# Kernel optimization log

Measured on AMD Instinct MI355X. Metric: run time of the kernel, lower is better.

The kernel has to match this reference:

```python
import jax, jax.numpy as jnp
import numpy as np

N_HEADS = 8
BUCKET = 64
EPS = 1e-4


def setup_inputs() -> dict:
    key = jax.random.key(0)
    ks = jax.random.split(key, 8)
    B, S, D = 4, 8192, 1024
    s = 1.0 / np.sqrt(D).astype(np.float32)
    x = jax.random.normal(ks[0], (B, S, D), dtype=jnp.float32)
    W_hash = jax.random.normal(ks[1], (D, 2 * N_HEADS), dtype=jnp.float32) * s
    W_q = jax.random.normal(ks[2], (D, D), dtype=jnp.float32) * s
    b_q = jax.random.normal(ks[3], (D,), dtype=jnp.float32) * 0.01
    W_v = jax.random.normal(ks[4], (D, D), dtype=jnp.float32) * s
    b_v = jax.random.normal(ks[5], (D,), dtype=jnp.float32) * 0.01
    W_o = jax.random.normal(ks[6], (D, D), dtype=jnp.float32) * s
    b_o = jax.random.normal(ks[7], (D,), dtype=jnp.float32) * 0.01
    return {"x": x, "W_hash": W_hash, "W_q": W_q, "b_q": b_q,
            "W_v": W_v, "b_v": b_v, "W_o": W_o, "b_o": b_o}


def reference(x, W_hash, W_q, b_q, W_v, b_v, W_o, b_o):
    B, S, D = x.shape
    H, dh = N_HEADS, D // N_HEADS
    nb = S // BUCKET  # number of LSH buckets per head

    # --- LSH hash: one angle per head, sort tokens by angle (per head) ---
    h = (x @ W_hash).reshape(B, S, H, 2)
    angles = h[..., 0] / (h[..., 1] + EPS)          # [B, S, H]
    idx = jnp.argsort(angles.transpose(0, 2, 1), axis=2)  # [B, H, S]

    # --- projections (shared_qk: k uses the same projection as q) ---
    q = x @ W_q + b_q
    k = q
    v = x @ W_v + b_v

    def to_heads(t):
        return t.reshape(B, S, H, dh).transpose(0, 2, 1, 3)  # [B, H, S, dh]

    qh, kh, vh = to_heads(q), to_heads(k), to_heads(v)

    gather = lambda t: jnp.take_along_axis(t, idx[..., None], axis=2)
    qs = gather(qh).reshape(B, H, nb, BUCKET, dh)
    ks = gather(kh).reshape(B, H, nb, BUCKET, dh)
    vs = gather(vh).reshape(B, H, nb, BUCKET, dh)

    # --- bucketed local attention ---
    scale = 1.0 / np.sqrt(dh).astype(np.float32)
    scores = jnp.einsum('bhnid,bhnjd->bhnij', qs, ks) * scale
    attn = jax.nn.softmax(scores, axis=-1)
    o = jnp.einsum('bhnij,bhnjd->bhnid', attn, vs).reshape(B, H, S, dh)

    # --- unsort back to original token order ---
    inv = jnp.argsort(idx, axis=2)                  # inverse permutation [B, H, S]
    o = jnp.take_along_axis(o, inv[..., None], axis=2)
    o = o.transpose(0, 2, 1, 3).reshape(B, S, D)
    return o @ W_o + b_o
```

## Files before the change

kernel.cpp:

```cpp
#include <hip/hip_runtime.h>

typedef unsigned short u16;
using short8 = __attribute__((ext_vector_type(8))) short;
using u16x8  = __attribute__((ext_vector_type(8))) unsigned short;
using f32x4  = __attribute__((ext_vector_type(4))) float;

#define B_   4
#define S_   8192
#define D_   1024
#define H_   8
#define DH_  128
#define NB_  128
#define M_   (B_ * S_)

static __device__ __forceinline__ float bf2f(u16 u) {
  union { unsigned int i; float f; } v; v.i = ((unsigned int)u) << 16; return v.f;
}
static __device__ __forceinline__ u16 f2bf(float f) {
  unsigned int x = __float_as_uint(f);
  unsigned int r = (x + 0x7fffu + ((x >> 16) & 1u)) >> 16;
  return (u16)r;
}
static __device__ __forceinline__ f32x4 mfma16(short8 a, short8 b, f32x4 c) {
  return __builtin_amdgcn_mfma_f32_16x16x32_bf16(a, b, c, 0, 0, 0);
}
static __device__ __forceinline__ void gload16(const u16* g, u16* l) {
  __builtin_amdgcn_global_load_lds(
      (const __attribute__((address_space(1))) void*)g,
      (__attribute__((address_space(3))) void*)l, 16, 0, 0);
}

__global__ __launch_bounds__(256) void cvt_k(const float* __restrict__ src,
                                             u16* __restrict__ dst) {
  const size_t i = ((size_t)blockIdx.x * 256 + threadIdx.x) * 8;
  const f32x4 a = *(const f32x4*)(src + i);
  const f32x4 b = *(const f32x4*)(src + i + 4);
  u16x8 r;
  r[0] = f2bf(a[0]); r[1] = f2bf(a[1]); r[2] = f2bf(a[2]); r[3] = f2bf(a[3]);
  r[4] = f2bf(b[0]); r[5] = f2bf(b[1]); r[6] = f2bf(b[2]); r[7] = f2bf(b[3]);
  *(u16x8*)(dst + i) = r;
}

__global__ __launch_bounds__(256) void transpose_k(const float* __restrict__ src,
                                                   u16* __restrict__ dst) {
  __shared__ float tile[32][33];
  const int bx = blockIdx.x * 32, by = blockIdx.y * 32;
  const int tx = threadIdx.x, ty = threadIdx.y;
#pragma unroll
  for (int i = ty; i < 32; i += 8) tile[i][tx] = src[(size_t)(by + i) * D_ + bx + tx];
  __syncthreads();
#pragma unroll
  for (int i = ty; i < 32; i += 8) dst[(size_t)(bx + i) * D_ + by + tx] = f2bf(tile[tx][i]);
}

__global__ __launch_bounds__(128) void angles_k(const float* __restrict__ x,
                                                const float* __restrict__ Wh,
                                                float* __restrict__ angles) {
  __shared__ float wsh[D_ * 16];
  const int tid = threadIdx.x;
  for (int i = tid; i < D_ * 16; i += 128) wsh[i] = Wh[i];
  __syncthreads();
  const int token = blockIdx.x * 128 + tid;
  const float* xr = x + (size_t)token * D_;
  f32x4 acc4[4];
#pragma unroll
  for (int i = 0; i < 4; i++) acc4[i] = 0.0f;
  for (int d0 = 0; d0 < D_; d0 += 4) {
    const f32x4 pk = *(const f32x4*)(xr + d0);
#pragma unroll
    for (int j = 0; j < 4; j++) {
      const float xv = pk[j];
      const f32x4* wr = (const f32x4*)&wsh[(d0 + j) * 16];
#pragma unroll
      for (int c4 = 0; c4 < 4; c4++) acc4[c4] += wr[c4] * xv;
    }
  }
  const int b = token >> 13, s = token & (S_ - 1);
#pragma unroll
  for (int h = 0; h < H_; h++) {
    const float num = acc4[h >> 1][(h & 1) * 2 + 0];
    const float den = acc4[h >> 1][(h & 1) * 2 + 1];
    angles[(size_t)(b * H_ + h) * S_ + s] = num / (den + 1e-4f);
  }
}

__global__ __launch_bounds__(1024) void sort_k(const float* __restrict__ angles,
                                               int* __restrict__ idx) {
  __shared__ float key[S_];
  __shared__ int   val[S_];
  const float* a = angles + (size_t)blockIdx.x * S_;
  const int tid = threadIdx.x;
  for (int i = tid; i < S_; i += 1024) { key[i] = a[i]; val[i] = i; }
  __syncthreads();
  for (int k = 2; k <= S_; k <<= 1) {
    for (int j = k >> 1; j > 0; j >>= 1) {
      for (int i = tid; i < S_; i += 1024) {
        const int ixj = i ^ j;
        if (ixj > i) {
          const float ki = key[i], kj = key[ixj];
          const bool up = (i & k) == 0;
          if (up ? (ki > kj) : (ki < kj)) {
            key[i] = kj; key[ixj] = ki;
            const int t = val[i]; val[i] = val[ixj]; val[ixj] = t;
          }
        }
      }
      __syncthreads();
    }
  }
  int* out = idx + (size_t)blockIdx.x * S_;
  for (int i = tid; i < S_; i += 1024) out[i] = val[i];
}

template <bool CF32>
__global__ __launch_bounds__(256) void gemm_bt(const u16* __restrict__ A,
                                               const u16* __restrict__ Bt,
                                               const float* __restrict__ bias,
                                               void* __restrict__ Cv,
                                               int M, int N, int K) {
  __shared__ __attribute__((aligned(16))) u16 As[128][32];
  __shared__ __attribute__((aligned(16))) u16 Bs[128][32];
  const int tid = threadIdx.x;
  const int wave = tid >> 6, lane = tid & 63;
  const int l16 = lane & 15, quad = lane >> 4;
  const int m0 = blockIdx.x * 128, n0 = blockIdx.y * 128;
  const int wm = wave >> 1, wn = wave & 1;
  const int srow = lane >> 2;
  const int scol = (lane & 3) * 8;

  const u16* Ag0 = A  + (size_t)(m0 + wave * 16 + srow) * K + scol;
  const u16* Ag1 = A  + (size_t)(m0 + 64 + wave * 16 + srow) * K + scol;
  const u16* Bg0 = Bt + (size_t)(n0 + wave * 16 + srow) * K + scol;
  const u16* Bg1 = Bt + (size_t)(n0 + 64 + wave * 16 + srow) * K + scol;
  u16* AsD0 = &As[wave * 16 + srow][scol];
  u16* AsD1 = &As[64 + wave * 16 + srow][scol];
  u16* BsD0 = &Bs[wave * 16 + srow][scol];
  u16* BsD1 = &Bs[64 + wave * 16 + srow][scol];

  f32x4 acc[4][4];
#pragma unroll
  for (int i = 0; i < 4; i++)
#pragma unroll
    for (int j = 0; j < 4; j++) acc[i][j] = 0.0f;

  for (int k0 = 0; k0 < K; k0 += 32) {
    __syncthreads();
    gload16(Ag0 + k0, AsD0);
    gload16(Ag1 + k0, AsD1);
    gload16(Bg0 + k0, BsD0);
    gload16(Bg1 + k0, BsD1);
    __syncthreads();
    short8 af[4], bfr[4];
#pragma unroll
    for (int i = 0; i < 4; i++)
      af[i] = *(const short8*)&As[wm * 64 + i * 16 + l16][quad * 8];
#pragma unroll
    for (int i = 0; i < 4; i++)
      bfr[i] = *(const short8*)&Bs[wn * 64 + i * 16 + l16][quad * 8];
#pragma unroll
    for (int mi = 0; mi < 4; mi++)
#pragma unroll
      for (int ni = 0; ni < 4; ni++)
        acc[mi][ni] = mfma16(af[mi], bfr[ni], acc[mi][ni]);
  }

#pragma unroll
  for (int ni = 0; ni < 4; ni++) {
    const int col = n0 + wn * 64 + ni * 16 + l16;
    const float bv = bias[col];
#pragma unroll
    for (int mi = 0; mi < 4; mi++) {
      const int rowb = m0 + wm * 64 + mi * 16 + quad * 4;
#pragma unroll
      for (int r = 0; r < 4; r++) {
        const float cv = acc[mi][ni][r] + bv;
        if (CF32) ((float*)Cv)[(size_t)(rowb + r) * N + col] = cv;
        else      ((u16*)Cv)[(size_t)(rowb + r) * N + col] = f2bf(cv);
      }
    }
  }
}

__global__ __launch_bounds__(256) void attn_k(const u16* __restrict__ qbuf,
                                              const u16* __restrict__ vbuf,
                                              const int* __restrict__ idx,
                                              u16* __restrict__ obuf) {
  __shared__ u16  Qs[64][136];
  __shared__ u16  Vt[128][72];
  __shared__ float Ss[64][65];
  __shared__ u16  Ps[64][72];
  __shared__ int  tids[64];
  const int b = blockIdx.z, h = blockIdx.y, n = blockIdx.x;
  const int tid = threadIdx.x;
  const int lane = tid & 63, wave = tid >> 6;
  const int l16 = lane & 15, quad = lane >> 4;

  if (tid < 64) tids[tid] = idx[(size_t)(b * H_ + h) * S_ + n * 64 + tid];
  __syncthreads();

  {
    const int i = tid & 63, seg = tid >> 6;
    const size_t rowoff = (size_t)(b * S_ + tids[i]) * D_ + h * DH_ + seg * 32;
    const u16* qr = qbuf + rowoff;
    const u16* vr = vbuf + rowoff;
#pragma unroll
    for (int c = 0; c < 32; c += 8)
      *(u16x8*)&Qs[i][seg * 32 + c] = *(const u16x8*)(qr + c);
#pragma unroll
    for (int c = 0; c < 32; c += 8) {
      u16x8 pv = *(const u16x8*)(vr + c);
#pragma unroll
      for (int j = 0; j < 8; j++) Vt[seg * 32 + c + j][i] = pv[j];
    }
  }
  __syncthreads();

  f32x4 sacc[4];
#pragma unroll
  for (int i = 0; i < 4; i++) sacc[i] = 0.0f;
#pragma unroll
  for (int k0 = 0; k0 < DH_; k0 += 32) {
    const short8 af = *(const short8*)&Qs[wave * 16 + l16][k0 + quad * 8];
#pragma unroll
    for (int ni = 0; ni < 4; ni++) {
      const short8 bfr = *(const short8*)&Qs[ni * 16 + l16][k0 + quad * 8];
      sacc[ni] = mfma16(af, bfr, sacc[ni]);
    }
  }
  const float scale = 0.08838834764831845f;
#pragma unroll
  for (int ni = 0; ni < 4; ni++)
#pragma unroll
    for (int r = 0; r < 4; r++)
      Ss[wave * 16 + quad * 4 + r][ni * 16 + l16] = sacc[ni][r] * scale;
  __syncthreads();

  {
    const int row = tid >> 2, part = tid & 3;
    float e[16]; float mx = -3.0e38f;
#pragma unroll
    for (int c = 0; c < 16; c++) { e[c] = Ss[row][part * 16 + c]; mx = fmaxf(mx, e[c]); }
    mx = fmaxf(mx, __shfl_xor(mx, 1));
    mx = fmaxf(mx, __shfl_xor(mx, 2));
    float sum = 0.f;
#pragma unroll
    for (int c = 0; c < 16; c++) { e[c] = __expf(e[c] - mx); sum += e[c]; }
    sum += __shfl_xor(sum, 1);
    sum += __shfl_xor(sum, 2);
    const float inv = 1.0f / sum;
#pragma unroll
    for (int c = 0; c < 16; c++) Ps[row][part * 16 + c] = f2bf(e[c] * inv);
  }
  __syncthreads();

  f32x4 oacc[8];
#pragma unroll
  for (int i = 0; i < 8; i++) oacc[i] = 0.0f;
#pragma unroll
  for (int k0 = 0; k0 < 64; k0 += 32) {
    const short8 pf = *(const short8*)&Ps[wave * 16 + l16][k0 + quad * 8];
#pragma unroll
    for (int nt = 0; nt < 8; nt++) {
      const short8 vf = *(const short8*)&Vt[nt * 16 + l16][k0 + quad * 8];
      oacc[nt] = mfma16(pf, vf, oacc[nt]);
    }
  }

  u16 (*Os)[128] = (u16(*)[128])&Ss[0][0];
#pragma unroll
  for (int r = 0; r < 4; r++) {
    const int m = wave * 16 + quad * 4 + r;
    const int swz = ((m >> 2) & 3) * 32;
#pragma unroll
    for (int nt = 0; nt < 8; nt++) Os[m][(nt * 16 + l16) ^ swz] = f2bf(oacc[nt][r]);
  }
  __syncthreads();

  {
    const int row = tid >> 2, c0 = (tid & 3) * 32;
    const int swz = ((row >> 2) & 3) * 32;
    u16* orow = obuf + (size_t)(b * S_ + tids[row]) * D_ + h * DH_ + c0;
#pragma unroll
    for (int c = 0; c < 32; c += 8)
      *(u16x8*)(orow + c) = *(const u16x8*)&Os[row][(c0 + c) ^ swz];
  }
}

extern "C" void kernel_launch(void* const* d_in, const int* in_sizes, int n_in,
                              void* d_out, int out_size, void* d_ws, size_t ws_size,
                              hipStream_t stream) {
  const float* x  = (const float*)d_in[0];
  const float* Wh = (const float*)d_in[1];
  const float* Wq = (const float*)d_in[2];
  const float* bq = (const float*)d_in[3];
  const float* Wv = (const float*)d_in[4];
  const float* bv = (const float*)d_in[5];
  const float* Wo = (const float*)d_in[6];
  const float* bo = (const float*)d_in[7];
  char* ws = (char*)d_ws;
  u16*   Wqt    = (u16*)(ws);
  u16*   Wvt    = (u16*)(ws + (2u << 20));
  u16*   Wot    = (u16*)(ws + (4u << 20));
  float* angles = (float*)(ws + (6u << 20));
  int*   idxb   = (int*)(ws + (7u << 20));
  u16*   qbuf   = (u16*)(ws + (8u << 20));
  u16*   xbf    = (u16*)d_out;
  u16*   vbuf   = (u16*)((char*)d_out + (64u << 20));
  float* out    = (float*)d_out;

  cvt_k<<<dim3(M_ * D_ / (256 * 8), 1, 1), dim3(256, 1, 1), 0, stream>>>(x, xbf);
  transpose_k<<<dim3(32, 32, 1), dim3(32, 8, 1), 0, stream>>>(Wq, Wqt);
  transpose_k<<<dim3(32, 32, 1), dim3(32, 8, 1), 0, stream>>>(Wv, Wvt);
  transpose_k<<<dim3(32, 32, 1), dim3(32, 8, 1), 0, stream>>>(Wo, Wot);
  angles_k<<<dim3(M_ / 128, 1, 1), dim3(128, 1, 1), 0, stream>>>(x, Wh, angles);
  sort_k<<<dim3(B_ * H_, 1, 1), dim3(1024, 1, 1), 0, stream>>>(angles, idxb);
  gemm_bt<false><<<dim3(M_ / 128, D_ / 128, 1), dim3(256, 1, 1), 0, stream>>>(xbf, Wqt, bq, qbuf, M_, D_, D_);
  gemm_bt<false><<<dim3(M_ / 128, D_ / 128, 1), dim3(256, 1, 1), 0, stream>>>(xbf, Wvt, bv, vbuf, M_, D_, D_);
  attn_k<<<dim3(NB_, H_, B_), dim3(256, 1, 1), 0, stream>>>(qbuf, vbuf, idxb, qbuf);
  gemm_bt<true><<<dim3(M_ / 128, D_ / 128, 1), dim3(256, 1, 1), 0, stream>>>(qbuf, Wot, bo, out, M_, D_, D_);
}
```

Baseline: 824.1 us.

## Split per-sequence bitonic sort into chunked shared-memory and global merge passes

Replaces the single-block-per-sequence bitonic sort (32 blocks of 1024 threads) with a multi-kernel bitonic sort. Packed 64-bit keys hold an order-preserving transformed angle in the high bits and the token index in the low bits. Chunks of 2048 are sorted in shared memory across 128 blocks, with global passes for the large strides. This raises parallelism, since the old sort used only 32 CUs, and removes the branchy key/value swap loops. The cost is extra kernel launches and global-memory round trips, and the key buffer is aliased into the output region.

Result: faster. 708.4 us (-14.0%).

```diff
diff --git a/kernel.cpp b/kernel.cpp
--- a/kernel.cpp
+++ b/kernel.cpp
@@ -1,6 +1,7 @@
 #include <hip/hip_runtime.h>
 
 typedef unsigned short u16;
+typedef unsigned long long u64;
 using short8 = __attribute__((ext_vector_type(8))) short;
 using u16x8  = __attribute__((ext_vector_type(8))) unsigned short;
 using f32x4  = __attribute__((ext_vector_type(4))) float;
@@ -53,9 +54,9 @@
   for (int i = ty; i < 32; i += 8) dst[(size_t)(bx + i) * D_ + by + tx] = f2bf(tile[tx][i]);
 }
 
-__global__ __launch_bounds__(128) void angles_k(const float* __restrict__ x,
-                                                const float* __restrict__ Wh,
-                                                float* __restrict__ angles) {
+__global__ __launch_bounds__(128) void keys_k(const float* __restrict__ x,
+                                              const float* __restrict__ Wh,
+                                              u64* __restrict__ keys) {
   __shared__ float wsh[D_ * 16];
   const int tid = threadIdx.x;
   for (int i = tid; i < D_ * 16; i += 128) wsh[i] = Wh[i];
@@ -80,36 +81,69 @@
   for (int h = 0; h < H_; h++) {
     const float num = acc4[h >> 1][(h & 1) * 2 + 0];
     const float den = acc4[h >> 1][(h & 1) * 2 + 1];
-    angles[(size_t)(b * H_ + h) * S_ + s] = num / (den + 1e-4f);
-  }
-}
-
-__global__ __launch_bounds__(1024) void sort_k(const float* __restrict__ angles,
-                                               int* __restrict__ idx) {
-  __shared__ float key[S_];
-  __shared__ int   val[S_];
-  const float* a = angles + (size_t)blockIdx.x * S_;
-  const int tid = threadIdx.x;
-  for (int i = tid; i < S_; i += 1024) { key[i] = a[i]; val[i] = i; }
-  __syncthreads();
-  for (int k = 2; k <= S_; k <<= 1) {
+    const float ang = num / (den + 1e-4f);
+    unsigned int ub = __float_as_uint(ang);
+    ub = (ub & 0x80000000u) ? ~ub : (ub | 0x80000000u);
+    keys[(size_t)(b * H_ + h) * S_ + s] = ((u64)ub << 32) | (unsigned int)s;
+  }
+}
+
+
+__global__ __launch_bounds__(1024) void sortA_k(u64* __restrict__ keys) {
+  __shared__ u64 ks[2048];
+  const int seq = blockIdx.y, chunk = blockIdx.x, t = threadIdx.x;
+  u64* g = keys + ((size_t)seq << 13) + (chunk << 11);
+  ks[t] = g[t]; ks[t + 1024] = g[t + 1024];
+  __syncthreads();
+  const int gbase = chunk << 11;
+  for (int k = 2; k <= 2048; k <<= 1) {
     for (int j = k >> 1; j > 0; j >>= 1) {
-      for (int i = tid; i < S_; i += 1024) {
-        const int ixj = i ^ j;
-        if (ixj > i) {
-          const float ki = key[i], kj = key[ixj];
-          const bool up = (i & k) == 0;
-          if (up ? (ki > kj) : (ki < kj)) {
-            key[i] = kj; key[ixj] = ki;
-            const int t = val[i]; val[i] = val[ixj]; val[ixj] = t;
-          }
-        }
-      }
+      const int i = ((t & ~(j - 1)) << 1) | (t & (j - 1));
+      const int p = i | j;
+      const bool up = ((gbase + i) & k) == 0;
+      const u64 a = ks[i], b = ks[p];
+      if ((a > b) == up) { ks[i] = b; ks[p] = a; }
       __syncthreads();
     }
   }
-  int* out = idx + (size_t)blockIdx.x * S_;
-  for (int i = tid; i < S_; i += 1024) out[i] = val[i];
+  g[t] = ks[t]; g[t + 1024] = ks[t + 1024];
+}
+
+__global__ __launch_bounds__(256) void sortG_k(u64* __restrict__ keys, int j, int k) {
+  const int p = blockIdx.x * 256 + threadIdx.x;
+  const int seq = p >> 12, q = p & 4095;
+  const int i = ((q & ~(j - 1)) << 1) | (q & (j - 1));
+  u64* g = keys + ((size_t)seq << 13);
+  const bool up = ((i & k) == 0);
+  const u64 a = g[i], b = g[i | j];
+  if ((a > b) == up) { g[i] = b; g[i | j] = a; }
+}
+
+template <int K, bool FINAL>
+__global__ __launch_bounds__(1024) void sortB_k(u64* __restrict__ keys,
+                                                int* __restrict__ idx) {
+  __shared__ u64 ks[2048];
+  const int seq = blockIdx.y, chunk = blockIdx.x, t = threadIdx.x;
+  u64* g = keys + ((size_t)seq << 13) + (chunk << 11);
+  ks[t] = g[t]; ks[t + 1024] = g[t + 1024];
+  __syncthreads();
+  const int gbase = chunk << 11;
+#pragma unroll
+  for (int j = 1024; j > 0; j >>= 1) {
+    const int i = ((t & ~(j - 1)) << 1) | (t & (j - 1));
+    const int p = i | j;
+    const bool up = ((gbase + i) & K) == 0;
+    const u64 a = ks[i], b = ks[p];
+    if ((a > b) == up) { ks[i] = b; ks[p] = a; }
+    __syncthreads();
+  }
+  if (FINAL) {
+    int* o = idx + ((size_t)seq << 13) + (chunk << 11);
+    o[t] = (int)(unsigned int)ks[t];
+    o[t + 1024] = (int)(unsigned int)ks[t + 1024];
+  } else {
+    g[t] = ks[t]; g[t + 1024] = ks[t + 1024];
+  }
 }
 
 template <bool CF32>
@@ -301,19 +335,24 @@
   u16*   Wqt    = (u16*)(ws);
   u16*   Wvt    = (u16*)(ws + (2u << 20));
   u16*   Wot    = (u16*)(ws + (4u << 20));
-  float* angles = (float*)(ws + (6u << 20));
   int*   idxb   = (int*)(ws + (7u << 20));
   u16*   qbuf   = (u16*)(ws + (8u << 20));
   u16*   xbf    = (u16*)d_out;
   u16*   vbuf   = (u16*)((char*)d_out + (64u << 20));
+  u64*   keys   = (u64*)((char*)d_out + (64u << 20));
   float* out    = (float*)d_out;
 
   cvt_k<<<dim3(M_ * D_ / (256 * 8), 1, 1), dim3(256, 1, 1), 0, stream>>>(x, xbf);
   transpose_k<<<dim3(32, 32, 1), dim3(32, 8, 1), 0, stream>>>(Wq, Wqt);
   transpose_k<<<dim3(32, 32, 1), dim3(32, 8, 1), 0, stream>>>(Wv, Wvt);
   transpose_k<<<dim3(32, 32, 1), dim3(32, 8, 1), 0, stream>>>(Wo, Wot);
-  angles_k<<<dim3(M_ / 128, 1, 1), dim3(128, 1, 1), 0, stream>>>(x, Wh, angles);
-  sort_k<<<dim3(B_ * H_, 1, 1), dim3(1024, 1, 1), 0, stream>>>(angles, idxb);
+  keys_k<<<dim3(M_ / 128, 1, 1), dim3(128, 1, 1), 0, stream>>>(x, Wh, keys);
+  sortA_k<<<dim3(4, 32, 1), dim3(1024, 1, 1), 0, stream>>>(keys);
+  sortG_k<<<dim3(512, 1, 1), dim3(256, 1, 1), 0, stream>>>(keys, 2048, 4096);
+  sortB_k<4096, false><<<dim3(4, 32, 1), dim3(1024, 1, 1), 0, stream>>>(keys, idxb);
+  sortG_k<<<dim3(512, 1, 1), dim3(256, 1, 1), 0, stream>>>(keys, 4096, 8192);
+  sortG_k<<<dim3(512, 1, 1), dim3(256, 1, 1), 0, stream>>>(keys, 2048, 8192);
+  sortB_k<8192, true><<<dim3(4, 32, 1), dim3(1024, 1, 1), 0, stream>>>(keys, idxb);
   gemm_bt<false><<<dim3(M_ / 128, D_ / 128, 1), dim3(256, 1, 1), 0, stream>>>(xbf, Wqt, bq, qbuf, M_, D_, D_);
   gemm_bt<false><<<dim3(M_ / 128, D_ / 128, 1), dim3(256, 1, 1), 0, stream>>>(xbf, Wvt, bv, vbuf, M_, D_, D_);
   attn_k<<<dim3(NB_, H_, B_), dim3(256, 1, 1), 0, stream>>>(qbuf, vbuf, idxb, qbuf);
```
